# Performance work log

Measured on AMD Instinct MI355X. Metric: run time of the kernel, lower is better.

## Reference

```python
import jax, jax.numpy as jnp
import numpy as np

EPS_NORM = 1e-12  # torch F.normalize default eps
EPS_Z = 1e-6
RATE = 0.999      # moving_average_rate
ALPHA = 4.0


def _l2norm(x):
    n = jnp.linalg.norm(x, axis=-1, keepdims=True)
    return x / jnp.maximum(n, EPS_NORM)


def _safe_pow(base, p):
    # base >= 0 (post-ReLU); avoid nan grads of 0**p by masking
    b = jnp.where(base > 0, base, 1.0)
    return jnp.where(base > 0, b ** p, 0.0)


def setup_inputs() -> dict:
    key = jax.random.key(0)
    ks = jax.random.split(key, 6)
    B, C, H, W, K = 8, 256, 64, 64, 1024
    return {
        "x": jax.random.normal(ks[0], (B, C, H, W), jnp.float32),
        "units_w": jax.random.normal(ks[1], (K, C), jnp.float32) * 0.02,
        "power": jnp.zeros((C,), jnp.float32),
        "g_w": jax.random.normal(ks[2], (C, C), jnp.float32) * (C ** -0.5),
        "g_b": jnp.zeros((C,), jnp.float32),
        "dwc_w": jax.random.normal(ks[3], (C, 1, 3, 3), jnp.float32) * (1.0 / 3.0),
        "dwc_b": jnp.zeros((C,), jnp.float32),
    }


def reference(x, units_w, power, g_w, g_b, dwc_w, dwc_b):
    b, c, h, w = x.shape
    kdim = units_w.shape[0]
    p = 1.0 + ALPHA * jax.nn.sigmoid(power)              # (c,)
    xf = jnp.transpose(x, (0, 2, 3, 1)).reshape(-1, c)   # (n,c)
    n = xf.shape[0]
    g = xf @ g_w.T + g_b                                 # (n,c)

    m = jax.lax.stop_gradient(units_w)                   # torch uses .data (detached)
    xn = _l2norm(xf)
    mn = _l2norm(m)
    score = xn @ mn.T                                    # (n,k) cosine similarity

    # EMA codebook update (update_flag=True path)
    xd = jax.lax.stop_gradient(xf)
    ind = jnp.argmax(score, axis=1)                      # (n,)
    counts = jax.ops.segment_sum(jnp.ones((n,), xd.dtype), ind, num_segments=kdim)
    sums = jax.ops.segment_sum(xd, ind, num_segments=kdim)  # (k,c)
    embed_mean = sums / (counts[:, None] + EPS_Z)
    m = m * RATE + embed_mean * (1.0 - RATE)
    mn = _l2norm(m)

    # power-kernel feature maps
    q_pos = _safe_pow(jax.nn.relu(xn), p)
    q_neg = _safe_pow(jax.nn.relu(-xn), p)
    k_pos = _safe_pow(jax.nn.relu(mn), p)
    k_neg = _safe_pow(jax.nn.relu(-mn), p)
    q_sim = jnp.concatenate([q_pos, q_neg], axis=-1)     # (n,2c)
    q_opp = jnp.concatenate([q_neg, q_pos], axis=-1)     # (n,2c)
    kk = jnp.concatenate([k_pos, k_neg], axis=-1)        # (k,2c)
    v1, v2 = jnp.split(m, 2, axis=-1)                    # (k,c/2) each
    kmean = kk.mean(axis=0)                              # (2c,)
    s = n ** -0.5

    z = 1.0 / (q_sim @ kmean + EPS_Z)                    # (n,)
    kv = (kk.T * s) @ (v1 * s)                           # (2c,c/2)
    x_sim = (q_sim @ kv) * z[:, None]                    # (n,c/2)

    z2 = 1.0 / (q_opp @ kmean + EPS_Z)
    kv2 = (kk.T * s) @ (v2 * s)
    x_opp = (q_opp @ kv2) * z2[:, None]

    xo = jnp.concatenate([x_sim, x_opp], axis=-1)        # (n,c)
    g4 = g.reshape(b, h, w, c).transpose(0, 3, 1, 2)     # (b,c,h,w)
    out = xo.reshape(b, h, w, c).transpose(0, 3, 1, 2)   # (b,c,h,w)

    conv = jax.lax.conv_general_dilated(
        out, dwc_w, window_strides=(1, 1), padding="SAME",
        feature_group_count=c,
        dimension_numbers=("NCHW", "OIHW", "NCHW")) + dwc_b[None, :, None, None]
    out = (out + conv) * g4
    return out, score
```

## Files before the change

kernel.cpp:

```cpp
#include <hip/hip_runtime.h>
#include <math.h>

#define BB 8
#define CC 256
#define HWHW 4096
#define NN 32768
#define KD 1024
#define C2 512

#define OFF_XF     0u
#define OFF_GT     8388608u
#define OFF_RNORM  16777216u
#define OFF_P      16809984u
#define OFF_MN0    16810240u
#define OFF_MNEW   17072384u
#define OFF_SUMS   17334528u
#define OFF_COUNTS 17596672u
#define OFF_KMEAN  17597696u
#define OFF_KVBIG  17598208u
#define OFF_Z      17729280u
#define OFF_Z2     17762048u
#define OFF_IND    17794816u
#define OFF_KK     17827584u
#define OFF_GWS    18351872u
#define OFF_KVS    18417408u
#define ZERO_CNT   394752u

typedef unsigned short u16;
typedef __attribute__((ext_vector_type(4))) unsigned short us4;
typedef __attribute__((ext_vector_type(8))) short s8;
typedef __attribute__((ext_vector_type(4))) float fx4;

__device__ __forceinline__ float wredsum(float v) {
#pragma unroll
  for (int o = 32; o; o >>= 1) v += __shfl_xor(v, o);
  return v;
}

__device__ __forceinline__ float fpow(float b, float p) {
  return __builtin_amdgcn_exp2f(p * __builtin_amdgcn_logf(b));
}

__device__ __forceinline__ u16 bf16h(float f) {
  unsigned u = __float_as_uint(f);
  return (u16)((u + 0x7FFFu + ((u >> 16) & 1u)) >> 16);
}
__device__ __forceinline__ void split1(float f, u16& h, u16& l) {
  u16 hh = bf16h(f);
  float hf = __uint_as_float(((unsigned)hh) << 16);
  h = hh;
  l = bf16h(f - hf);
}
__device__ __forceinline__ void split4(float a0, float a1, float a2, float a3,
                                       us4& hv, us4& lv) {
  u16 h0, l0, h1, l1, h2, l2, h3, l3;
  split1(a0, h0, l0); split1(a1, h1, l1);
  split1(a2, h2, l2); split1(a3, h3, l3);
  hv = (us4){h0, h1, h2, h3};
  lv = (us4){l0, l1, l2, l3};
}

__device__ __forceinline__ void stage_pre(u16* __restrict__ H, u16* __restrict__ L,
                                          int kc, int row, us4 hv, us4 lv) {
  int g = kc & 3;
  int off = g * 1024 + (((row + 2 * g) & 127) << 3) + ((kc >> 2) << 2);
  *(us4*)(H + off) = hv;
  *(us4*)(L + off) = lv;
}
__device__ __forceinline__ void stage_pair(u16* __restrict__ H, u16* __restrict__ L,
                                           int kc, int row,
                                           float a0, float a1, float a2, float a3) {
  us4 hv, lv;
  split4(a0, a1, a2, a3, hv, lv);
  stage_pre(H, L, kc, row, hv, lv);
}
__device__ __forceinline__ s8 fragld(const u16* __restrict__ M, int g, int r) {
  return *(const s8*)(M + g * 1024 + (((r + 2 * g) & 127) << 3));
}
#define MFMA(a, b, c) __builtin_amdgcn_mfma_f32_16x16x32_bf16((a), (b), (c), 0, 0, 0)

__global__ void k_prep(const float* __restrict__ power, float* __restrict__ p) {
  int i = threadIdx.x;
  p[i] = 1.0f + 4.0f / (1.0f + expf(-power[i]));
}

__global__ void k_zero(float* __restrict__ zr) {
  unsigned i = blockIdx.x * 256u + threadIdx.x;
  if (i < ZERO_CNT) zr[i] = 0.0f;
}

__global__ void k_splitbuf(const float* __restrict__ src, u16* __restrict__ h,
                           u16* __restrict__ l, int n4) {
  int i = blockIdx.x * 256 + threadIdx.x;
  if (i >= n4) return;
  float4 v = *(const float4*)(src + (size_t)i * 4);
  us4 hv, lv;
  split4(v.x, v.y, v.z, v.w, hv, lv);
  *(us4*)(h + (size_t)i * 4) = hv;
  *(us4*)(l + (size_t)i * 4) = lv;
}

__global__ void k_transpose(const float* __restrict__ x, float* __restrict__ xf) {
  __shared__ float tile[32][33];
  int b = blockIdx.z, hw0 = blockIdx.x * 32, c0 = blockIdx.y * 32;
  int tx = threadIdx.x, ty = threadIdx.y;
#pragma unroll
  for (int i = 0; i < 32; i += 8)
    tile[ty + i][tx] = x[(size_t)(b * CC + c0 + ty + i) * HWHW + hw0 + tx];
  __syncthreads();
#pragma unroll
  for (int i = 0; i < 32; i += 8)
    xf[(size_t)(b * HWHW + hw0 + ty + i) * CC + c0 + tx] = tile[tx][ty + i];
}

__global__ void k_rownorm(const float* __restrict__ xf, float* __restrict__ rnorm) {
  int wv = threadIdx.x >> 6, ln = threadIdx.x & 63;
  int row = blockIdx.x * 4 + wv;
  float4 v = *(const float4*)(xf + (size_t)row * CC + ln * 4);
  float ss = wredsum(v.x * v.x + v.y * v.y + v.z * v.z + v.w * v.w);
  if (ln == 0) rnorm[row] = 1.0f / fmaxf(sqrtf(ss), 1e-12f);
}

__global__ void k_mnorm(const float* __restrict__ uw, u16* __restrict__ mh,
                        u16* __restrict__ ml) {
  int wv = threadIdx.x >> 6, ln = threadIdx.x & 63;
  int row = blockIdx.x * 4 + wv;
  float4 v = *(const float4*)(uw + (size_t)row * CC + ln * 4);
  float ss = wredsum(v.x * v.x + v.y * v.y + v.z * v.z + v.w * v.w);
  float rn = 1.0f / fmaxf(sqrtf(ss), 1e-12f);
  us4 hv, lv;
  split4(v.x * rn, v.y * rn, v.z * rn, v.w * rn, hv, lv);
  *(us4*)(mh + (size_t)row * CC + ln * 4) = hv;
  *(us4*)(ml + (size_t)row * CC + ln * 4) = lv;
}

__global__ __launch_bounds__(256) void k_score_mfma(const float* __restrict__ xf,
                                                    const float* __restrict__ rnorm,
                                                    const u16* __restrict__ mh,
                                                    const u16* __restrict__ ml,
                                                    float* __restrict__ score) {
  __shared__ __align__(16) u16 Lds[4][4096];
  u16 *Ah = Lds[0], *Al = Lds[1], *Bh = Lds[2], *Bl = Lds[3];
  int t = threadIdx.x, w = t >> 6, l = t & 63;
  int wr = w >> 1, wc = w & 1;
  int kc = t & 7, lr = t >> 3;
  int row0 = blockIdx.x * 128, col0 = blockIdx.y * 128;
  fx4 acc[4][4];
#pragma unroll
  for (int i = 0; i < 4; i++)
#pragma unroll
    for (int j = 0; j < 4; j++) acc[i][j] = (fx4){0.f, 0.f, 0.f, 0.f};

  for (int k0 = 0; k0 < CC; k0 += 32) {
    __syncthreads();
#pragma unroll
    for (int ps = 0; ps < 4; ps++) {
      int row = lr + ps * 32;
      float4 va = *(const float4*)(xf + (size_t)(row0 + row) * CC + k0 + kc * 4);
      stage_pair(Ah, Al, kc, row, va.x, va.y, va.z, va.w);
      size_t bo = (size_t)(col0 + row) * CC + k0 + kc * 4;
      stage_pre(Bh, Bl, kc, row, *(const us4*)(mh + bo), *(const us4*)(ml + bo));
    }
    __syncthreads();
    int g = l >> 4, rl = l & 15;
    s8 ah[4], al4[4], bh[4], bl4[4];
#pragma unroll
    for (int i = 0; i < 4; i++) {
      ah[i]  = fragld(Ah, g, wr * 64 + i * 16 + rl);
      al4[i] = fragld(Al, g, wr * 64 + i * 16 + rl);
      bh[i]  = fragld(Bh, g, wc * 64 + i * 16 + rl);
      bl4[i] = fragld(Bl, g, wc * 64 + i * 16 + rl);
    }
#pragma unroll
    for (int i = 0; i < 4; i++)
#pragma unroll
      for (int j = 0; j < 4; j++) {
        acc[i][j] = MFMA(ah[i], bh[j], acc[i][j]);
        acc[i][j] = MFMA(ah[i], bl4[j], acc[i][j]);
        acc[i][j] = MFMA(al4[i], bh[j], acc[i][j]);
      }
  }
  int row_l = (l >> 4) * 4, col_l = l & 15;
#pragma unroll
  for (int i = 0; i < 4; i++) {
    int rbase = row0 + wr * 64 + i * 16 + row_l;
    float4 rn4 = *(const float4*)(rnorm + rbase);
    float rr[4] = {rn4.x, rn4.y, rn4.z, rn4.w};
#pragma unroll
    for (int j = 0; j < 4; j++) {
      int col = col0 + wc * 64 + j * 16 + col_l;
#pragma unroll
      for (int reg = 0; reg < 4; reg++)
        score[(size_t)(rbase + reg) * KD + col] = acc[i][j][reg] * rr[reg];
    }
  }
}

__global__ __launch_bounds__(256) void k_g_mfma(const float* __restrict__ xf,
                                                const u16* __restrict__ gwh,
                                                const u16* __restrict__ gwl,
                                                const float* __restrict__ gb,
                                                float* __restrict__ gt) {
  __shared__ __align__(16) u16 Lds[4][4096];
  u16 *Ah = Lds[0], *Al = Lds[1], *Bh = Lds[2], *Bl = Lds[3];
  int t = threadIdx.x, w = t >> 6, l = t & 63;
  int wr = w >> 1, wc = w & 1;
  int kc = t & 7, lr = t >> 3;
  int row0 = blockIdx.x * 128, col0 = blockIdx.y * 128;
  fx4 acc[4][4];
#pragma unroll
  for (int i = 0; i < 4; i++)
#pragma unroll
    for (int j = 0; j < 4; j++) acc[i][j] = (fx4){0.f, 0.f, 0.f, 0.f};

  for (int k0 = 0; k0 < CC; k0 += 32) {
    __syncthreads();
#pragma unroll
    for (int ps = 0; ps < 4; ps++) {
      int row = lr + ps * 32;
      float4 va = *(const float4*)(xf + (size_t)(row0 + row) * CC + k0 + kc * 4);
      stage_pair(Ah, Al, kc, row, va.x, va.y, va.z, va.w);
      size_t bo = (size_t)(col0 + row) * CC + k0 + kc * 4;
      stage_pre(Bh, Bl, kc, row, *(const us4*)(gwh + bo), *(const us4*)(gwl + bo));
    }
    __syncthreads();
    int g = l >> 4, rl = l & 15;
    s8 ah[4], al4[4], bh[4], bl4[4];
#pragma unroll
    for (int i = 0; i < 4; i++) {
      ah[i]  = fragld(Ah, g, wr * 64 + i * 16 + rl);
      al4[i] = fragld(Al, g, wr * 64 + i * 16 + rl);
      bh[i]  = fragld(Bh, g, wc * 64 + i * 16 + rl);
      bl4[i] = fragld(Bl, g, wc * 64 + i * 16 + rl);
    }
#pragma unroll
    for (int i = 0; i < 4; i++)
#pragma unroll
      for (int j = 0; j < 4; j++) {
        acc[i][j] = MFMA(ah[i], bh[j], acc[i][j]);
        acc[i][j] = MFMA(ah[i], bl4[j], acc[i][j]);
        acc[i][j] = MFMA(al4[i], bh[j], acc[i][j]);
      }
  }
  int row_l = (l >> 4) * 4, col_l = l & 15;
#pragma unroll
  for (int j = 0; j < 4; j++) {
    int col = col0 + wc * 64 + j * 16 + col_l;
    float gbv = gb[col];
#pragma unroll
    for (int i = 0; i < 4; i++) {
      int rbase = row0 + wr * 64 + i * 16 + row_l;
#pragma unroll
      for (int reg = 0; reg < 4; reg++) {
        int row = rbase + reg;
        int b = row >> 12, hw = row & 4095;
        gt[(size_t)(b * CC + col) * HWHW + hw] = acc[i][j][reg] + gbv;
      }
    }
  }
}

__global__ __launch_bounds__(256) void k_x_mfma(const float* __restrict__ xf,
                                                const float* __restrict__ rnorm,
                                                const float* __restrict__ p,
                                                const u16* __restrict__ kvh,
                                                const u16* __restrict__ kvl,
                                                const float* __restrict__ z,
                                                const float* __restrict__ z2,
                                                float* __restrict__ xot) {
  __shared__ __align__(16) u16 Lds[4][4096];
  u16 *Ah = Lds[0], *Al = Lds[1], *Bh = Lds[2], *Bl = Lds[3];
  int t = threadIdx.x, w = t >> 6, l = t & 63;
  int wr = w >> 1, wc = w & 1;
  int kc = t & 7, lr = t >> 3;
  int row0 = blockIdx.x * 128, col0 = blockIdx.y * 128;
  float rnA[4];
#pragma unroll
  for (int ps = 0; ps < 4; ps++) rnA[ps] = rnorm[row0 + lr + ps * 32];
  fx4 acc[4][4];
#pragma unroll
  for (int i = 0; i < 4; i++)
#pragma unroll
    for (int j = 0; j < 4; j++) acc[i][j] = (fx4){0.f, 0.f, 0.f, 0.f};

  for (int k0 = 0; k0 < C2; k0 += 32) {
    bool negh = (k0 >= 256);
    int c4 = (k0 & 255) + kc * 4;
    float4 p4 = *(const float4*)(p + c4);
    __syncthreads();
#pragma unroll
    for (int ps = 0; ps < 4; ps++) {
      int row = lr + ps * 32;
      float4 xv = *(const float4*)(xf + (size_t)(row0 + row) * CC + c4);
      float rn = rnA[ps];
      float b0 = negh ? -(xv.x * rn) : (xv.x * rn);
      float b1 = negh ? -(xv.y * rn) : (xv.y * rn);
      float b2 = negh ? -(xv.z * rn) : (xv.z * rn);
      float b3 = negh ? -(xv.w * rn) : (xv.w * rn);
      float q0 = b0 > 0.f ? fpow(b0, p4.x) : 0.f;
      float q1 = b1 > 0.f ? fpow(b1, p4.y) : 0.f;
      float q2 = b2 > 0.f ? fpow(b2, p4.z) : 0.f;
      float q3 = b3 > 0.f ? fpow(b3, p4.w) : 0.f;
      stage_pair(Ah, Al, kc, row, q0, q1, q2, q3);
      size_t bo = (size_t)(col0 + row) * C2 + k0 + kc * 4;
      stage_pre(Bh, Bl, kc, row, *(const us4*)(kvh + bo), *(const us4*)(kvl + bo));
    }
    __syncthreads();
    int g = l >> 4, rl = l & 15;
    s8 ah[4], al4[4], bh[4], bl4[4];
#pragma unroll
    for (int i = 0; i < 4; i++) {
      ah[i]  = fragld(Ah, g, wr * 64 + i * 16 + rl);
      al4[i] = fragld(Al, g, wr * 64 + i * 16 + rl);
      bh[i]  = fragld(Bh, g, wc * 64 + i * 16 + rl);
      bl4[i] = fragld(Bl, g, wc * 64 + i * 16 + rl);
    }
#pragma unroll
    for (int i = 0; i < 4; i++)
#pragma unroll
      for (int j = 0; j < 4; j++) {
        acc[i][j] = MFMA(ah[i], bh[j], acc[i][j]);
        acc[i][j] = MFMA(ah[i], bl4[j], acc[i][j]);
        acc[i][j] = MFMA(al4[i], bh[j], acc[i][j]);
      }
  }
  const float* zz = (col0 == 0) ? z : z2;
  int row_l = (l >> 4) * 4, col_l = l & 15;
#pragma unroll
  for (int i = 0; i < 4; i++) {
    int rbase = row0 + wr * 64 + i * 16 + row_l;
    float4 z4 = *(const float4*)(zz + rbase);
    float zr[4] = {z4.x, z4.y, z4.z, z4.w};
#pragma unroll
    for (int j = 0; j < 4; j++) {
      int col = col0 + wc * 64 + j * 16 + col_l;
#pragma unroll
      for (int reg = 0; reg < 4; reg++) {
        int row = rbase + reg;
        int b = row >> 12, hw = row & 4095;
        xot[(size_t)(b * CC + col) * HWHW + hw] = acc[i][j][reg] * zr[reg];
      }
    }
  }
}

__global__ void k_argmax(const float* __restrict__ score, int* __restrict__ ind) {
  int wv = threadIdx.x >> 6, ln = threadIdx.x & 63;
  int row = blockIdx.x * 4 + wv;
  const float* r = score + (size_t)row * KD;
  float best = -3.4e38f; int bi = 0;
#pragma unroll
  for (int ch = 0; ch < 4; ch++) {
    int base = ln * 16 + ch * 4;
    float4 v = *(const float4*)(r + base);
    float vv[4] = {v.x, v.y, v.z, v.w};
#pragma unroll
    for (int j = 0; j < 4; j++) {
      float val = vv[j]; int idx = base + j;
      if (val > best || (val == best && idx < bi)) { best = val; bi = idx; }
    }
  }
#pragma unroll
  for (int o = 32; o; o >>= 1) {
    float ov = __shfl_xor(best, o); int oi = __shfl_xor(bi, o);
    if (ov > best || (ov == best && oi < bi)) { best = ov; bi = oi; }
  }
  if (ln == 0) ind[row] = bi;
}

__global__ void k_scatter(const float* __restrict__ xf, const int* __restrict__ ind,
                          float* __restrict__ sums, float* __restrict__ counts) {
  int wv = threadIdx.x >> 6, ln = threadIdx.x & 63;
  int row = blockIdx.x * 4 + wv;
  int j = ind[row];
  const float* xr = xf + (size_t)row * CC;
  float* sb = sums + (size_t)j * CC;
#pragma unroll
  for (int c = 0; c < CC; c += 64) atomicAdd(&sb[c + ln], xr[c + ln]);
  if (ln == 0) atomicAdd(&counts[j], 1.0f);
}

__global__ void k_ema(const float* __restrict__ uw, const float* __restrict__ sums,
                      const float* __restrict__ counts, const float* __restrict__ p,
                      float* __restrict__ mnew, float* __restrict__ kkb) {
  int wv = threadIdx.x >> 6, ln = threadIdx.x & 63;
  int j = blockIdx.x * 4 + wv;
  int c = ln * 4;
  float cnt = counts[j] + 1e-6f;
  float4 s4 = *(const float4*)(sums + (size_t)j * CC + c);
  float4 u4 = *(const float4*)(uw + (size_t)j * CC + c);
  float4 m4;
  m4.x = u4.x * 0.999f + (s4.x / cnt) * 0.001f;
  m4.y = u4.y * 0.999f + (s4.y / cnt) * 0.001f;
  m4.z = u4.z * 0.999f + (s4.z / cnt) * 0.001f;
  m4.w = u4.w * 0.999f + (s4.w / cnt) * 0.001f;
  *(float4*)(mnew + (size_t)j * CC + c) = m4;
  float ss = wredsum(m4.x * m4.x + m4.y * m4.y + m4.z * m4.z + m4.w * m4.w);
  float rn = 1.0f / fmaxf(sqrtf(ss), 1e-12f);
  float4 p4 = *(const float4*)(p + c);
  float mv[4] = {m4.x * rn, m4.y * rn, m4.z * rn, m4.w * rn};
  float pv[4] = {p4.x, p4.y, p4.z, p4.w};
  float kp[4], kn[4];
#pragma unroll
  for (int i = 0; i < 4; i++) {
    kp[i] = mv[i] > 0.0f ? fpow(mv[i], pv[i]) : 0.0f;
    kn[i] = (-mv[i]) > 0.0f ? fpow(-mv[i], pv[i]) : 0.0f;
  }
  float4 kp4 = {kp[0], kp[1], kp[2], kp[3]};
  float4 kn4 = {kn[0], kn[1], kn[2], kn[3]};
  *(float4*)(kkb + (size_t)j * C2 + c) = kp4;
  *(float4*)(kkb + (size_t)j * C2 + 256 + c) = kn4;
}

__global__ void k_kmean(const float* __restrict__ kkb, float* __restrict__ kmean) {
  __shared__ float part[8][32];
  int cl = threadIdx.x & 31;
  int c = blockIdx.x * 32 + cl;
  int rc = threadIdx.x >> 5;
  float s = 0.f;
#pragma unroll 8
  for (int r = rc * 128; r < rc * 128 + 128; r++)
    s += kkb[(size_t)r * C2 + c];
  part[rc][cl] = s;
  __syncthreads();
  if (rc == 0) {
    float tsum = 0.f;
#pragma unroll
    for (int i = 0; i < 8; i++) tsum += part[i][cl];
    kmean[c] = tsum * (1.0f / 1024.0f);
  }
}

__global__ __launch_bounds__(256) void k_kv(const float* __restrict__ kkb,
                                            const float* __restrict__ mnew,
                                            float* __restrict__ kvT) {
  __shared__ float Ks[32][64];
  __shared__ float Ms[32][64];
  int t = threadIdx.x;
  int t0 = blockIdx.x * 64, c0 = blockIdx.y * 64, kbase = blockIdx.z * 128;
  int cl4 = (t & 15) * 4, kr = t >> 4;
  int fr = (t & 15) * 4, fc = ((t >> 4) & 15) * 4;
  float acc[4][4] = {};
  for (int k0 = kbase; k0 < kbase + 128; k0 += 32) {
    __syncthreads();
#pragma unroll
    for (int ps = 0; ps < 2; ps++) {
      int kr2 = kr + ps * 16;
      *(float4*)&Ks[kr2][cl4] = *(const float4*)(kkb + (size_t)(k0 + kr2) * C2 + t0 + cl4);
      *(float4*)&Ms[kr2][cl4] = *(const float4*)(mnew + (size_t)(k0 + kr2) * CC + c0 + cl4);
    }
    __syncthreads();
#pragma unroll
    for (int kx = 0; kx < 32; kx++) {
      float4 a = *(const float4*)&Ks[kx][fr];
      float4 b = *(const float4*)&Ms[kx][fc];
      float av[4] = {a.x, a.y, a.z, a.w}, bv[4] = {b.x, b.y, b.z, b.w};
#pragma unroll
      for (int i = 0; i < 4; i++)
#pragma unroll
        for (int j = 0; j < 4; j++) acc[i][j] += av[i] * bv[j];
    }
  }
  const float sc = 1.0f / 32768.0f;
#pragma unroll
  for (int i = 0; i < 4; i++) {
    int tt = t0 + fr + i;
#pragma unroll
    for (int j = 0; j < 4; j++) {
      int c = c0 + fc + j;
      int drow = (c < 128) ? tt : ((tt + 256) & 511);
      atomicAdd(&kvT[(size_t)c * C2 + drow], acc[i][j] * sc);
    }
  }
}

__global__ void k_z(const float* __restrict__ xf, const float* __restrict__ rnorm,
                    const float* __restrict__ p, const float* __restrict__ kmean,
                    float* __restrict__ z, float* __restrict__ z2) {
  int wv = threadIdx.x >> 6, ln = threadIdx.x & 63;
  int row = blockIdx.x * 4 + wv;
  int c = ln * 4;
  float rn = rnorm[row];
  float4 v = *(const float4*)(xf + (size_t)row * CC + c);
  float4 p4 = *(const float4*)(p + c);
  float4 k0 = *(const float4*)(kmean + c);
  float4 k1 = *(const float4*)(kmean + 256 + c);
  float xv[4] = {v.x * rn, v.y * rn, v.z * rn, v.w * rn};
  float pv[4] = {p4.x, p4.y, p4.z, p4.w};
  float ka[4] = {k0.x, k0.y, k0.z, k0.w};
  float kb[4] = {k1.x, k1.y, k1.z, k1.w};
  float za = 0.0f, zb = 0.0f;
#pragma unroll
  for (int i = 0; i < 4; i++) {
    float qp = xv[i] > 0.0f ? fpow(xv[i], pv[i]) : 0.0f;
    float qn = (-xv[i]) > 0.0f ? fpow(-xv[i], pv[i]) : 0.0f;
    za += qp * ka[i] + qn * kb[i];
    zb += qn * ka[i] + qp * kb[i];
  }
  za = wredsum(za); zb = wredsum(zb);
  if (ln == 0) { z[row] = 1.0f / (za + 1e-6f); z2[row] = 1.0f / (zb + 1e-6f); }
}

__global__ __launch_bounds__(256) void k_conv(float* __restrict__ out,
                                              const float* __restrict__ gt,
                                              const float* __restrict__ wc,
                                              const float* __restrict__ bc) {
  __shared__ float pl[64][64];
  int plane = blockIdx.x;
  int ch = plane & 255;
  int t = threadIdx.x;
  const float* src = out + (size_t)plane * HWHW;
#pragma unroll
  for (int ps = 0; ps < 4; ps++) {
    int i = ps * 1024 + t * 4;
    *(float4*)&pl[i >> 6][i & 63] = *(const float4*)(src + i);
  }
  float w[9];
#pragma unroll
  for (int i = 0; i < 9; i++) w[i] = wc[ch * 9 + i];
  float bias = bc[ch];
  __syncthreads();
#pragma unroll
  for (int ps = 0; ps < 16; ps++) {
    int pix = ps * 256 + t;
    int y = pix >> 6, x = pix & 63;
    float s = 0.0f;
#pragma unroll
    for (int dy = -1; dy <= 1; dy++) {
      int yy = y + dy;
      if (yy < 0 || yy > 63) continue;
#pragma unroll
      for (int dx = -1; dx <= 1; dx++) {
        int xx = x + dx;
        if (xx < 0 || xx > 63) continue;
        s += w[(dy + 1) * 3 + dx + 1] * pl[yy][xx];
      }
    }
    out[(size_t)plane * HWHW + pix] =
        (pl[y][x] + s + bias) * gt[(size_t)plane * HWHW + pix];
  }
}

extern "C" void kernel_launch(void* const* d_in, const int* in_sizes, int n_in,
                              void* d_out, int out_size, void* d_ws, size_t ws_size,
                              hipStream_t stream) {
  const float* x     = (const float*)d_in[0];
  const float* uw    = (const float*)d_in[1];
  const float* power = (const float*)d_in[2];
  const float* gw    = (const float*)d_in[3];
  const float* gb    = (const float*)d_in[4];
  const float* wc    = (const float*)d_in[5];
  const float* bcb   = (const float*)d_in[6];
  float* out   = (float*)d_out;
  float* score = out + (size_t)NN * CC;
  float* ws = (float*)d_ws;

  float* xf    = ws + OFF_XF;
  float* gt    = ws + OFF_GT;
  float* rnorm = ws + OFF_RNORM;
  float* p     = ws + OFF_P;
  u16*   mn0h  = (u16*)(ws + OFF_MN0);
  u16*   mn0l  = (u16*)(ws + OFF_MN0 + 131072);
  float* mnew  = ws + OFF_MNEW;
  float* sums  = ws + OFF_SUMS;
  float* cnts  = ws + OFF_COUNTS;
  float* kmean = ws + OFF_KMEAN;
  float* kvT   = ws + OFF_KVBIG;
  float* z     = ws + OFF_Z;
  float* z2    = ws + OFF_Z2;
  int*   ind   = (int*)(ws + OFF_IND);
  float* kkbuf = ws + OFF_KK;
  u16*   gwh   = (u16*)(ws + OFF_GWS);
  u16*   gwl   = (u16*)(ws + OFF_GWS + 32768);
  u16*   kvh   = (u16*)(ws + OFF_KVS);
  u16*   kvl   = (u16*)(ws + OFF_KVS + 65536);

  k_prep<<<1, 256, 0, stream>>>(power, p);
  k_zero<<<1542, 256, 0, stream>>>(sums);
  k_transpose<<<dim3(128, 8, 8), dim3(32, 8), 0, stream>>>(x, xf);
  k_rownorm<<<8192, 256, 0, stream>>>(xf, rnorm);
  k_mnorm<<<256, 256, 0, stream>>>(uw, mn0h, mn0l);
  k_splitbuf<<<64, 256, 0, stream>>>(gw, gwh, gwl, 16384);
  k_score_mfma<<<dim3(256, 8), 256, 0, stream>>>(xf, rnorm, mn0h, mn0l, score);
  k_g_mfma<<<dim3(256, 2), 256, 0, stream>>>(xf, gwh, gwl, gb, gt);
  k_argmax<<<8192, 256, 0, stream>>>(score, ind);
  k_scatter<<<8192, 256, 0, stream>>>(xf, ind, sums, cnts);
  k_ema<<<256, 256, 0, stream>>>(uw, sums, cnts, p, mnew, kkbuf);
  k_kmean<<<16, 256, 0, stream>>>(kkbuf, kmean);
  k_kv<<<dim3(8, 4, 8), 256, 0, stream>>>(kkbuf, mnew, kvT);
  k_splitbuf<<<128, 256, 0, stream>>>(kvT, kvh, kvl, 32768);
  k_z<<<8192, 256, 0, stream>>>(xf, rnorm, p, kmean, z, z2);
  k_x_mfma<<<dim3(256, 2), 256, 0, stream>>>(xf, rnorm, p, kvh, kvl, z, z2, out);
  k_conv<<<2048, 256, 0, stream>>>(out, gt, wc, bcb);
}
```

Baseline: 459.2 us.

## Fuse small kernels: merge argmax with scatter, prep with zero, kv with split

```diff
diff --git a/kernel.cpp b/kernel.cpp
--- a/kernel.cpp
+++ b/kernel.cpp
@@ -24,7 +24,7 @@
 #define OFF_KK     17827584u
 #define OFF_GWS    18351872u
 #define OFF_KVS    18417408u
-#define ZERO_CNT   394752u
+#define ZERO_CNT   263168u
 
 typedef unsigned short u16;
 typedef __attribute__((ext_vector_type(4))) unsigned short us4;
@@ -79,14 +79,12 @@
 }
 #define MFMA(a, b, c) __builtin_amdgcn_mfma_f32_16x16x32_bf16((a), (b), (c), 0, 0, 0)
 
-__global__ void k_prep(const float* __restrict__ power, float* __restrict__ p) {
-  int i = threadIdx.x;
-  p[i] = 1.0f + 4.0f / (1.0f + expf(-power[i]));
-}
-
-__global__ void k_zero(float* __restrict__ zr) {
+__global__ void k_zero(float* __restrict__ zr, const float* __restrict__ power,
+                       float* __restrict__ p) {
   unsigned i = blockIdx.x * 256u + threadIdx.x;
   if (i < ZERO_CNT) zr[i] = 0.0f;
+  if (blockIdx.x == 0)
+    p[threadIdx.x] = 1.0f + 4.0f / (1.0f + expf(-power[threadIdx.x]));
 }
 
 __global__ void k_splitbuf(const float* __restrict__ src, u16* __restrict__ h,
@@ -344,7 +342,8 @@
   }
 }
 
-__global__ void k_argmax(const float* __restrict__ score, int* __restrict__ ind) {
+__global__ void k_assign(const float* __restrict__ score, const float* __restrict__ xf,
+                         float* __restrict__ sums, float* __restrict__ counts) {
   int wv = threadIdx.x >> 6, ln = threadIdx.x & 63;
   int row = blockIdx.x * 4 + wv;
   const float* r = score + (size_t)row * KD;
@@ -365,14 +364,7 @@
     float ov = __shfl_xor(best, o); int oi = __shfl_xor(bi, o);
     if (ov > best || (ov == best && oi < bi)) { best = ov; bi = oi; }
   }
-  if (ln == 0) ind[row] = bi;
-}
-
-__global__ void k_scatter(const float* __restrict__ xf, const int* __restrict__ ind,
-                          float* __restrict__ sums, float* __restrict__ counts) {
-  int wv = threadIdx.x >> 6, ln = threadIdx.x & 63;
-  int row = blockIdx.x * 4 + wv;
-  int j = ind[row];
+  int j = bi;
   const float* xr = xf + (size_t)row * CC;
   float* sb = sums + (size_t)j * CC;
 #pragma unroll
@@ -433,15 +425,16 @@
 
 __global__ __launch_bounds__(256) void k_kv(const float* __restrict__ kkb,
                                             const float* __restrict__ mnew,
-                                            float* __restrict__ kvT) {
+                                            u16* __restrict__ kvh,
+                                            u16* __restrict__ kvl) {
   __shared__ float Ks[32][64];
   __shared__ float Ms[32][64];
   int t = threadIdx.x;
-  int t0 = blockIdx.x * 64, c0 = blockIdx.y * 64, kbase = blockIdx.z * 128;
+  int t0 = blockIdx.x * 64, c0 = blockIdx.y * 64;
   int cl4 = (t & 15) * 4, kr = t >> 4;
   int fr = (t & 15) * 4, fc = ((t >> 4) & 15) * 4;
   float acc[4][4] = {};
-  for (int k0 = kbase; k0 < kbase + 128; k0 += 32) {
+  for (int k0 = 0; k0 < KD; k0 += 32) {
     __syncthreads();
 #pragma unroll
     for (int ps = 0; ps < 2; ps++) {
@@ -469,7 +462,10 @@
     for (int j = 0; j < 4; j++) {
       int c = c0 + fc + j;
       int drow = (c < 128) ? tt : ((tt + 256) & 511);
-      atomicAdd(&kvT[(size_t)c * C2 + drow], acc[i][j] * sc);
+      u16 h, l;
+      split1(acc[i][j] * sc, h, l);
+      kvh[(size_t)c * C2 + drow] = h;
+      kvl[(size_t)c * C2 + drow] = l;
     }
   }
 }
@@ -565,30 +561,25 @@
   float* sums  = ws + OFF_SUMS;
   float* cnts  = ws + OFF_COUNTS;
   float* kmean = ws + OFF_KMEAN;
-  float* kvT   = ws + OFF_KVBIG;
   float* z     = ws + OFF_Z;
   float* z2    = ws + OFF_Z2;
-  int*   ind   = (int*)(ws + OFF_IND);
   float* kkbuf = ws + OFF_KK;
   u16*   gwh   = (u16*)(ws + OFF_GWS);
   u16*   gwl   = (u16*)(ws + OFF_GWS + 32768);
   u16*   kvh   = (u16*)(ws + OFF_KVS);
   u16*   kvl   = (u16*)(ws + OFF_KVS + 65536);
 
-  k_prep<<<1, 256, 0, stream>>>(power, p);
-  k_zero<<<1542, 256, 0, stream>>>(sums);
+  k_zero<<<1028, 256, 0, stream>>>(sums, power, p);
   k_transpose<<<dim3(128, 8, 8), dim3(32, 8), 0, stream>>>(x, xf);
   k_rownorm<<<8192, 256, 0, stream>>>(xf, rnorm);
   k_mnorm<<<256, 256, 0, stream>>>(uw, mn0h, mn0l);
   k_splitbuf<<<64, 256, 0, stream>>>(gw, gwh, gwl, 16384);
   k_score_mfma<<<dim3(256, 8), 256, 0, stream>>>(xf, rnorm, mn0h, mn0l, score);
   k_g_mfma<<<dim3(256, 2), 256, 0, stream>>>(xf, gwh, gwl, gb, gt);
-  k_argmax<<<8192, 256, 0, stream>>>(score, ind);
-  k_scatter<<<8192, 256, 0, stream>>>(xf, ind, sums, cnts);
+  k_assign<<<8192, 256, 0, stream>>>(score, xf, sums, cnts);
   k_ema<<<256, 256, 0, stream>>>(uw, sums, cnts, p, mnew, kkbuf);
   k_kmean<<<16, 256, 0, stream>>>(kkbuf, kmean);
-  k_kv<<<dim3(8, 4, 8), 256, 0, stream>>>(kkbuf, mnew, kvT);
-  k_splitbuf<<<128, 256, 0, stream>>>(kvT, kvh, kvl, 32768);
+  k_kv<<<dim3(8, 4), 256, 0, stream>>>(kkbuf, mnew, kvh, kvl);
   k_z<<<8192, 256, 0, stream>>>(xf, rnorm, p, kmean, z, z2);
   k_x_mfma<<<dim3(256, 2), 256, 0, stream>>>(xf, rnorm, p, kvh, kvl, z, z2, out);
   k_conv<<<2048, 256, 0, stream>>>(out, gt, wc, bcb);
```

Result: no change. 460.1 us (+0.2%).
